# Kernel tuning notes

Measured on AMD Instinct MI355X. Metric: run time of the kernel, lower is better.

## Reference

```python
import jax, jax.numpy as jnp
import numpy as np

IN_CH, OUT_CH, K = 3, 16, 3

def setup_inputs() -> dict:
    key = jax.random.key(0)
    kx, kw, kb = jax.random.split(key, 3)
    x = jax.random.normal(kx, (64, IN_CH, 256, 256), dtype=jnp.float32)
    # kaiming_uniform_(a=sqrt(5)) -> bound = sqrt(6 / ((1+5) * fan_in)) = 1/sqrt(fan_in)
    fan_in = IN_CH * K * K
    bound = 1.0 / np.sqrt(fan_in)
    weight = jax.random.uniform(kw, (OUT_CH, IN_CH, K, K), dtype=jnp.float32,
                                minval=-bound, maxval=bound)
    bias = jax.random.uniform(kb, (OUT_CH,), dtype=jnp.float32,
                              minval=-bound, maxval=bound)
    return {"x": x, "weight": weight, "bias": bias}

def reference(x, weight, bias):
    # stride 1, VALID padding conv2d (NCHW / OIHW), same math as the quadruple loop
    out = jax.lax.conv_general_dilated(
        x, weight,
        window_strides=(1, 1),
        padding="VALID",
        dimension_numbers=("NCHW", "OIHW", "NCHW"),
    )
    return out + bias[None, :, None, None]
```

## Files before the change

### kernel.cpp

```cpp
#include <hip/hip_runtime.h>


constexpr int N = 64, C = 3, H = 256, W = 256;
constexpr int OC = 16, K = 3, OH = 254, OW = 254;
constexpr int PW = OW / 2;

__global__ __launch_bounds__(256) void conv3x3_kernel(
    const float* __restrict__ x, const float* __restrict__ w,
    const float* __restrict__ bias, float* __restrict__ out)
{
    int idx = blockIdx.x * blockDim.x + threadIdx.x;
    constexpr int total = N * OH * PW;
    if (idx >= total) return;

    int pw = idx % PW;
    int t  = idx / PW;
    int oh = t % OH;
    int n  = t / OH;
    int ow = pw * 2;

    float acc0[OC], acc1[OC];
    #pragma unroll
    for (int oc = 0; oc < OC; ++oc) {
        float b = bias[oc];
        acc0[oc] = b;
        acc1[oc] = b;
    }

    const float* xb = x + (size_t)n * C * H * W;

    #pragma unroll
    for (int c = 0; c < C; ++c) {
        #pragma unroll
        for (int kh = 0; kh < K; ++kh) {
            const float* xr = xb + ((size_t)c * H + (oh + kh)) * W + ow;
            float i0 = xr[0], i1 = xr[1], i2 = xr[2], i3 = xr[3];
            #pragma unroll
            for (int oc = 0; oc < OC; ++oc) {
                float w0 = w[((oc * C + c) * K + kh) * K + 0];
                float w1 = w[((oc * C + c) * K + kh) * K + 1];
                float w2 = w[((oc * C + c) * K + kh) * K + 2];
                acc0[oc] += i0 * w0 + i1 * w1 + i2 * w2;
                acc1[oc] += i1 * w0 + i2 * w1 + i3 * w2;
            }
        }
    }

    float* ob = out + ((size_t)n * OC * OH + oh) * OW + ow;
    #pragma unroll
    for (int oc = 0; oc < OC; ++oc) {
        float2 v = make_float2(acc0[oc], acc1[oc]);
        *reinterpret_cast<float2*>(ob + (size_t)oc * OH * OW) = v;
    }
}

extern "C" void kernel_launch(void* const* d_in, const int* in_sizes, int n_in,
                              void* d_out, int out_size, void* d_ws, size_t ws_size,
                              hipStream_t stream) {
    const float* x    = (const float*)d_in[0];
    const float* w    = (const float*)d_in[1];
    const float* bias = (const float*)d_in[2];
    float* out        = (float*)d_out;

    constexpr int total  = N * OH * PW;
    constexpr int block  = 256;
    constexpr int blocks = (total + block - 1) / block;
    conv3x3_kernel<<<blocks, block, 0, stream>>>(x, w, bias, out);
}
```

Before: 329.2 us.

## Remap threads to four contiguous flat outputs with vectorized nontemporal stores

Each thread now computes four consecutive elements of the flat output (one output channel) instead of two pixels across all sixteen channels. This lets every thread write one aligned 16-byte nontemporal store, so the output writes form fully contiguous wavefront stores. Rows that wrap around are handled by a scalar fallback. The cost is that input rows are re-read once per output channel (relying on cache), along with per-thread index division and a divergent edge path.

```diff
diff --git a/kernel.cpp b/kernel.cpp
--- a/kernel.cpp
+++ b/kernel.cpp
@@ -3,55 +3,84 @@
 
 constexpr int N = 64, C = 3, H = 256, W = 256;
 constexpr int OC = 16, K = 3, OH = 254, OW = 254;
-constexpr int PW = OW / 2;
+constexpr unsigned TOTAL = (unsigned)N * OC * OH * OW;
+constexpr unsigned NTHREADS = TOTAL / 4;
+
+typedef float v4a4  __attribute__((ext_vector_type(4), aligned(4)));
+typedef float v2a4  __attribute__((ext_vector_type(2), aligned(4)));
+typedef float v4a16 __attribute__((ext_vector_type(4), aligned(16)));
 
 __global__ __launch_bounds__(256) void conv3x3_kernel(
     const float* __restrict__ x, const float* __restrict__ w,
     const float* __restrict__ bias, float* __restrict__ out)
 {
-    int idx = blockIdx.x * blockDim.x + threadIdx.x;
-    constexpr int total = N * OH * PW;
-    if (idx >= total) return;
+    unsigned idx = blockIdx.x * 256u + threadIdx.x;
+    if (idx >= NTHREADS) return;
+    unsigned f = idx * 4u;
 
-    int pw = idx % PW;
-    int t  = idx / PW;
-    int oh = t % OH;
-    int n  = t / OH;
-    int ow = pw * 2;
+    unsigned q   = f / OW;
+    int      ow0 = (int)(f - q * OW);
+    int      oh  = (int)(q % OH);
+    unsigned t2  = q / OH;
+    int      oc  = (int)(t2 & 15u);
+    int      nIm = (int)(t2 >> 4);
 
-    float acc0[OC], acc1[OC];
-    #pragma unroll
-    for (int oc = 0; oc < OC; ++oc) {
+    float av[4];
+
+    if (ow0 <= OW - 4) {
+        const float* xb = x + (size_t)nIm * C * H * W;
+        const float* wp = w + oc * (C * K * K);
         float b = bias[oc];
-        acc0[oc] = b;
-        acc1[oc] = b;
-    }
-
-    const float* xb = x + (size_t)n * C * H * W;
-
-    #pragma unroll
-    for (int c = 0; c < C; ++c) {
+        float a0 = b, a1 = b, a2 = b, a3 = b;
         #pragma unroll
-        for (int kh = 0; kh < K; ++kh) {
-            const float* xr = xb + ((size_t)c * H + (oh + kh)) * W + ow;
-            float i0 = xr[0], i1 = xr[1], i2 = xr[2], i3 = xr[3];
+        for (int c = 0; c < C; ++c) {
+            const float* wc = wp + c * 9;
+            v4a4 wA = *reinterpret_cast<const v4a4*>(wc);
+            v4a4 wB = *reinterpret_cast<const v4a4*>(wc + 4);
+            float w8 = wc[8];
+            float wk[9] = {wA.x, wA.y, wA.z, wA.w, wB.x, wB.y, wB.z, wB.w, w8};
             #pragma unroll
-            for (int oc = 0; oc < OC; ++oc) {
-                float w0 = w[((oc * C + c) * K + kh) * K + 0];
-                float w1 = w[((oc * C + c) * K + kh) * K + 1];
-                float w2 = w[((oc * C + c) * K + kh) * K + 2];
-                acc0[oc] += i0 * w0 + i1 * w1 + i2 * w2;
-                acc1[oc] += i1 * w0 + i2 * w1 + i3 * w2;
+            for (int kh = 0; kh < K; ++kh) {
+                const float* xr = xb + ((size_t)c * H + (oh + kh)) * W + ow0;
+                v4a4 lo = *reinterpret_cast<const v4a4*>(xr);
+                v2a4 hi = *reinterpret_cast<const v2a4*>(xr + 4);
+                float w0 = wk[kh * 3 + 0];
+                float w1 = wk[kh * 3 + 1];
+                float w2 = wk[kh * 3 + 2];
+                a0 += lo.x * w0 + lo.y * w1 + lo.z * w2;
+                a1 += lo.y * w0 + lo.z * w1 + lo.w * w2;
+                a2 += lo.z * w0 + lo.w * w1 + hi.x * w2;
+                a3 += lo.w * w0 + hi.x * w1 + hi.y * w2;
             }
+        }
+        av[0] = a0; av[1] = a1; av[2] = a2; av[3] = a3;
+    } else {
+        #pragma unroll
+        for (int p = 0; p < 4; ++p) {
+            unsigned g  = f + p;
+            unsigned qq = g / OW;
+            int oww = (int)(g - qq * OW);
+            int ohh = (int)(qq % OH);
+            unsigned tt = qq / OH;
+            int occ = (int)(tt & 15u);
+            int nn  = (int)(tt >> 4);
+            const float* xbp = x + (size_t)nn * C * H * W;
+            const float* wpp = w + occ * (C * K * K);
+            float acc = bias[occ];
+            #pragma unroll
+            for (int c = 0; c < C; ++c)
+                #pragma unroll
+                for (int kh = 0; kh < K; ++kh) {
+                    const float* xr = xbp + ((size_t)c * H + (ohh + kh)) * W + oww;
+                    const float* wc = wpp + (c * K + kh) * K;
+                    acc += xr[0] * wc[0] + xr[1] * wc[1] + xr[2] * wc[2];
+                }
+            av[p] = acc;
         }
     }
 
-    float* ob = out + ((size_t)n * OC * OH + oh) * OW + ow;
-    #pragma unroll
-    for (int oc = 0; oc < OC; ++oc) {
-        float2 v = make_float2(acc0[oc], acc1[oc]);
-        *reinterpret_cast<float2*>(ob + (size_t)oc * OH * OW) = v;
-    }
+    v4a16 v = {av[0], av[1], av[2], av[3]};
+    __builtin_nontemporal_store(v, reinterpret_cast<v4a16*>(out + f));
 }
 
 extern "C" void kernel_launch(void* const* d_in, const int* in_sizes, int n_in,
@@ -62,8 +91,6 @@
     const float* bias = (const float*)d_in[2];
     float* out        = (float*)d_out;
 
-    constexpr int total  = N * OH * PW;
-    constexpr int block  = 256;
-    constexpr int blocks = (total + block - 1) / block;
-    conv3x3_kernel<<<blocks, block, 0, stream>>>(x, w, bias, out);
+    constexpr unsigned blocks = NTHREADS / 256u;
+    conv3x3_kernel<<<blocks, 256, 0, stream>>>(x, w, bias, out);
 }
```

Measured after the change: 668.4 us. 2.03x slower.
